# Performance work log

Measured on AMD Instinct MI355X. Metric: run time of the kernel, lower is better.

The kernel has to match this reference:

```python
import jax, jax.numpy as jnp
import numpy as np

DIM = 768
N_HEADS = 12
HEAD_DIM = DIM // N_HEADS  # 64
SEQ = 4096
ROPE_THETA = 10000.0  # local layer (layer_id=1)
WINDOW = 128          # local_attention; mask is distance <= WINDOW // 2


def setup_inputs() -> dict:
    key = jax.random.key(0)
    k1, k2, k3 = jax.random.split(key, 3)
    x = jax.random.normal(k1, (1, SEQ, DIM), dtype=jnp.float32)
    position_ids = jnp.arange(SEQ, dtype=jnp.int64 if jax.config.jax_enable_x64 else jnp.int32).reshape(1, SEQ)
    wqkv = jax.random.normal(k2, (3 * DIM, DIM), dtype=jnp.float32) * 0.02
    wo = jax.random.normal(k3, (DIM, DIM), dtype=jnp.float32) * 0.02
    return {"x": x, "position_ids": position_ids, "wqkv": wqkv, "wo": wo}


def _rope_cos_sin(position_ids):
    # inv_freq over even dims, freqs duplicated to full head_dim
    inv_freq = 1.0 / (ROPE_THETA ** (jnp.arange(0, HEAD_DIM, 2, dtype=jnp.float32) / HEAD_DIM))
    pos = position_ids.reshape(-1).astype(jnp.float32)           # [S]
    freqs = pos[:, None] * inv_freq[None, :]                      # [S, hd/2]
    freqs = jnp.concatenate([freqs, freqs], axis=-1)              # [S, hd]
    return jnp.cos(freqs)[None, None], jnp.sin(freqs)[None, None]  # [1,1,S,hd]


def _rotate_half(t):
    h = t.shape[-1] // 2
    return jnp.concatenate([-t[..., h:], t[..., :h]], axis=-1)


def reference(x, position_ids, wqkv, wo):
    bsz, seq_len, _ = x.shape
    qkv = jnp.einsum("bsd,ed->bse", x, wqkv)                      # [B,S,3*dim]
    qkv = qkv.reshape(bsz, seq_len, 3, N_HEADS, HEAD_DIM)
    qkv = jnp.transpose(qkv, (0, 3, 2, 1, 4))                      # [B,H,3,S,hd]
    q, k, v = qkv[:, :, 0], qkv[:, :, 1], qkv[:, :, 2]             # [B,H,S,hd]

    cos, sin = _rope_cos_sin(position_ids)
    q = q * cos + _rotate_half(q) * sin
    k = k * cos + _rotate_half(k) * sin

    scale = HEAD_DIM ** -0.5
    scores = jnp.einsum("bhqd,bhkd->bhqk", q, k) * scale           # [B,H,S,S]

    # sliding-window mask: |i - j| <= WINDOW // 2
    idx = jnp.arange(seq_len)
    dist = jnp.abs(idx[None, :] - idx[:, None])                    # [S,S]
    window_mask = dist <= (WINDOW // 2)
    scores = jnp.where(window_mask[None, None], scores, -jnp.inf)

    attn = jax.nn.softmax(scores, axis=-1)
    out = jnp.einsum("bhqk,bhkd->bhqd", attn, v)                   # [B,H,S,hd]
    out = jnp.transpose(out, (0, 2, 1, 3)).reshape(bsz, seq_len, DIM)
    out = jnp.einsum("bsd,ed->bse", out, wo)
    return out
```

## Files before the change

### kernel.cpp

```cpp
#include <hip/hip_runtime.h>
#include <math.h>

#define SEQ 4096
#define DIM 768
#define NH 12
#define HD 64
#define QKV_N 2304
#define HALF_WIN 64

typedef __attribute__((ext_vector_type(8))) short bf16x8;
typedef __attribute__((ext_vector_type(4))) float floatx4;

__device__ __forceinline__ unsigned short f2bf(float f) {
    unsigned u = __float_as_uint(f);
    unsigned r = (u + 0x7fffu + ((u >> 16) & 1u)) >> 16;
    return (unsigned short)r;
}

__device__ __forceinline__ void gld16(const void* g, void* l) {
    __builtin_amdgcn_global_load_lds(
        (const __attribute__((address_space(1))) unsigned*)g,
        (__attribute__((address_space(3))) unsigned*)l, 16, 0, 0);
}

__device__ __forceinline__ void fast_sc(float x, float* s, float* c) {
    float r = x * 0.15915494309189535f;
    r = r - floorf(r);
    *s = __builtin_amdgcn_sinf(r);
    *c = __builtin_amdgcn_cosf(r);
}

__global__ __launch_bounds__(256) void cast3_bf16(const float* __restrict__ x,
                                                  const float* __restrict__ wqkv,
                                                  const float* __restrict__ wo,
                                                  unsigned short* __restrict__ dst,
                                                  int nx4, int nw4, int ntot4) {
    int i = blockIdx.x * 256 + threadIdx.x;
    if (i >= ntot4) return;
    const float4* src;
    int off;
    if (i < nx4)            { src = (const float4*)x;    off = i; }
    else if (i < nx4 + nw4) { src = (const float4*)wqkv; off = i - nx4; }
    else                    { src = (const float4*)wo;   off = i - nx4 - nw4; }
    float4 v = src[off];
    ushort4 r;
    r.x = f2bf(v.x); r.y = f2bf(v.y); r.z = f2bf(v.z); r.w = f2bf(v.w);
    *(ushort4*)(dst + (size_t)i * 4) = r;
}

__global__ __launch_bounds__(256) void gemm_qkv_rope(const unsigned short* __restrict__ A,
                                                     const unsigned short* __restrict__ B,
                                                     unsigned short* __restrict__ qr,
                                                     unsigned short* __restrict__ kr,
                                                     unsigned short* __restrict__ vt) {
    __shared__ __align__(16) short smem[32768];
    const int t  = threadIdx.x;
    const int wv = t >> 6, ln = t & 63;
    const int wm = wv >> 1, wn = wv & 1;
    const int bm0 = blockIdx.y * 128;
    const int bn0 = blockIdx.x * 128;
    const int lrow = ln >> 3;
    const int lu   = ln & 7;
    const int frow = ln & 15;
    const int q    = ln >> 4;
    const int K = DIM;

    const unsigned short* gptr[8];
    int loff[8];
#pragma unroll
    for (int i = 0; i < 8; i++) {
        int idx = wv * 8 + i;
        int c   = (idx < 16) ? idx : idx - 16;
        int row = c * 8 + lrow;
        int g   = (lu ^ (row & 7)) << 3;
        if (idx < 16) {
            gptr[i] = A + (size_t)(bm0 + row) * K + g;
            loff[i] = c * 512;
        } else {
            gptr[i] = B + (size_t)(bn0 + row) * K + g;
            loff[i] = 8192 + c * 512;
        }
    }

    floatx4 acc[4][4];
#pragma unroll
    for (int i = 0; i < 4; i++)
#pragma unroll
        for (int j = 0; j < 4; j++) acc[i][j] = (floatx4){0.f, 0.f, 0.f, 0.f};

#pragma unroll
    for (int i = 0; i < 8; i++) gld16(gptr[i], (void*)(smem + loff[i]));
    __syncthreads();

    int cur = 0;
    for (int it = 0; it < 12; it++) {
        if (it + 1 < 12) {
            int nb = cur ^ 1;
            int k0n = (it + 1) * 64;
#pragma unroll
            for (int i = 0; i < 8; i++)
                gld16(gptr[i] + k0n, (void*)(smem + nb * 16384 + loff[i]));
        }
        short* As = smem + cur * 16384;
        short* Bs = As + 8192;
#pragma unroll
        for (int ks = 0; ks < 2; ks++) {
            bf16x8 af[4], bfr[4];
#pragma unroll
            for (int mt = 0; mt < 4; mt++) {
                int ra = wm * 64 + mt * 16 + frow;
                af[mt] = *(const bf16x8*)&As[ra * 64 + (((ks * 4 + q) ^ (ra & 7)) << 3)];
            }
#pragma unroll
            for (int nt = 0; nt < 4; nt++) {
                int rb = wn * 64 + nt * 16 + frow;
                bfr[nt] = *(const bf16x8*)&Bs[rb * 64 + (((ks * 4 + q) ^ (rb & 7)) << 3)];
            }
#pragma unroll
            for (int mt = 0; mt < 4; mt++)
#pragma unroll
                for (int nt = 0; nt < 4; nt++)
                    acc[mt][nt] = __builtin_amdgcn_mfma_f32_16x16x32_bf16(
                        af[mt], bfr[nt], acc[mt][nt], 0, 0, 0);
        }
        __syncthreads();
        cur ^= 1;
    }

    const int cn = frow;
    const int part = (bn0 >= 1536) ? 2 : (bn0 >= 768 ? 1 : 0);

    if (part < 2) {
        const int wcol = bn0 - part * 768 + wn * 64;
        const int h = wcol >> 6;
        unsigned short* dst = (part == 0 ? qr : kr) + (size_t)h * SEQ * HD;
        const float invf0 = exp2f(-(float)cn * 0.4152410118609203f);
        const float invf1 = exp2f(-(float)(cn + 16) * 0.4152410118609203f);
#pragma unroll
        for (int mt = 0; mt < 4; mt++) {
            const int sbase = bm0 + wm * 64 + mt * 16 + q * 4;
#pragma unroll
            for (int r = 0; r < 4; r++) {
                float ss = (float)(sbase + r);
                float sn0, cs0, sn1, cs1;
                fast_sc(ss * invf0, &sn0, &cs0);
                fast_sc(ss * invf1, &sn1, &cs1);
                float o0 = acc[mt][0][r] * cs0 - acc[mt][2][r] * sn0;
                float o1 = acc[mt][1][r] * cs1 - acc[mt][3][r] * sn1;
                float o2 = acc[mt][2][r] * cs0 + acc[mt][0][r] * sn0;
                float o3 = acc[mt][3][r] * cs1 + acc[mt][1][r] * sn1;
                unsigned short* p = dst + (size_t)(sbase + r) * HD + cn;
                p[0]  = f2bf(o0);
                p[16] = f2bf(o1);
                p[32] = f2bf(o2);
                p[48] = f2bf(o3);
            }
        }
    } else {
        short* vstage = smem + wv * 4608;
#pragma unroll
        for (int mt = 0; mt < 4; mt++) {
#pragma unroll
            for (int nt = 0; nt < 4; nt++) {
                int d    = nt * 16 + cn;
                int sloc = mt * 16 + q * 4;
                ushort4 pk;
                pk.x = f2bf(acc[mt][nt][0]);
                pk.y = f2bf(acc[mt][nt][1]);
                pk.z = f2bf(acc[mt][nt][2]);
                pk.w = f2bf(acc[mt][nt][3]);
                *(ushort4*)&vstage[d * 72 + sloc] = pk;
            }
        }
        __syncthreads();
#pragma unroll
        for (int itr = 0; itr < 8; itr++) {
            int dr = (t >> 4) + itr * 16;
            int u  = t & 15;
            int region = ((u >> 3) << 1) | (dr >> 6);
            uint4 val = *(const uint4*)&smem[region * 4608 + (dr & 63) * 72 + (u & 7) * 8];
            unsigned short* vp = vt + (size_t)(bn0 - 1536 + dr) * SEQ + bm0 + u * 8;
            *(uint4*)vp = val;
        }
    }
}

__global__ __launch_bounds__(256) void gemm_out(const unsigned short* __restrict__ A,
                                                const unsigned short* __restrict__ B,
                                                float* __restrict__ C,
                                                int M, int N, int K) {
    __shared__ __align__(16) short smem[16384];
    const int t  = threadIdx.x;
    const int wv = t >> 6, ln = t & 63;
    const int wm = wv >> 1, wn = wv & 1;
    const int bm0 = blockIdx.y * 64;
    const int bn0 = blockIdx.x * 64;
    const int lrow = ln >> 3;
    const int lu   = ln & 7;
    const int frow = ln & 15;
    const int q    = ln >> 4;

    const unsigned short* gptr[4];
    int loff[4];
#pragma unroll
    for (int i = 0; i < 4; i++) {
        int idx = wv * 4 + i;
        int c   = (idx < 8) ? idx : idx - 8;
        int row = c * 8 + lrow;
        int g   = (lu ^ (row & 7)) << 3;
        if (idx < 8) {
            gptr[i] = A + (size_t)(bm0 + row) * K + g;
            loff[i] = c * 512;
        } else {
            gptr[i] = B + (size_t)(bn0 + row) * K + g;
            loff[i] = 4096 + c * 512;
        }
    }

    floatx4 acc[2][2];
#pragma unroll
    for (int i = 0; i < 2; i++)
#pragma unroll
        for (int j = 0; j < 2; j++) acc[i][j] = (floatx4){0.f, 0.f, 0.f, 0.f};

#pragma unroll
    for (int i = 0; i < 4; i++) gld16(gptr[i], (void*)(smem + loff[i]));
    __syncthreads();

    int cur = 0;
    const int NIT = K / 64;
    for (int it = 0; it < NIT; it++) {
        if (it + 1 < NIT) {
            int nb = cur ^ 1;
            int k0n = (it + 1) * 64;
#pragma unroll
            for (int i = 0; i < 4; i++)
                gld16(gptr[i] + k0n, (void*)(smem + nb * 8192 + loff[i]));
        }
        short* As = smem + cur * 8192;
        short* Bs = As + 4096;
#pragma unroll
        for (int ks = 0; ks < 2; ks++) {
            bf16x8 af[2], bfr[2];
#pragma unroll
            for (int mt = 0; mt < 2; mt++) {
                int ra = wm * 32 + mt * 16 + frow;
                af[mt] = *(const bf16x8*)&As[ra * 64 + (((ks * 4 + q) ^ (ra & 7)) << 3)];
            }
#pragma unroll
            for (int nt = 0; nt < 2; nt++) {
                int rb = wn * 32 + nt * 16 + frow;
                bfr[nt] = *(const bf16x8*)&Bs[rb * 64 + (((ks * 4 + q) ^ (rb & 7)) << 3)];
            }
#pragma unroll
            for (int mt = 0; mt < 2; mt++)
#pragma unroll
                for (int nt = 0; nt < 2; nt++)
                    acc[mt][nt] = __builtin_amdgcn_mfma_f32_16x16x32_bf16(
                        af[mt], bfr[nt], acc[mt][nt], 0, 0, 0);
        }
        __syncthreads();
        cur ^= 1;
    }

    const int cn = ln & 15;
    const int rb4 = (ln >> 4) * 4;
#pragma unroll
    for (int mt = 0; mt < 2; mt++) {
#pragma unroll
        for (int nt = 0; nt < 2; nt++) {
            floatx4 v = acc[mt][nt];
            float* cp = C + (size_t)(bm0 + wm * 32 + mt * 16 + rb4) * N +
                        bn0 + wn * 32 + nt * 16 + cn;
#pragma unroll
            for (int r = 0; r < 4; r++) cp[(size_t)r * N] = v[r];
        }
    }
}

__global__ __launch_bounds__(512) void attn_mfma(const unsigned short* __restrict__ Q,
                                                 const unsigned short* __restrict__ K,
                                                 const unsigned short* __restrict__ Vt,
                                                 unsigned short* __restrict__ Out) {
    __shared__ __align__(16) short lds[16384];
    short* Ks  = lds;
    short* Vts = lds + 4096;
    short* Pb  = lds + 8192;
    const int t  = threadIdx.x;
    const int wv = t >> 6, ln = t & 63;
    const int h  = blockIdx.x, qs = blockIdx.y * 128;
    const int frow = ln & 15, qd = ln >> 4;
    const int rl = ln >> 3, uu = ln & 7;
    const unsigned short* Qh = Q + (size_t)h * SEQ * HD;
    const unsigned short* Kh = K + (size_t)h * SEQ * HD;
    const unsigned short* Vh = Vt + (size_t)h * HD * SEQ;

    const unsigned short* qp = Qh + (size_t)(qs + wv * 16 + frow) * HD;
    bf16x8 af0 = *(const bf16x8*)(qp + qd * 8);
    bf16x8 af1 = *(const bf16x8*)(qp + (qd + 4) * 8);

    floatx4 accO[4];
#pragma unroll
    for (int i = 0; i < 4; i++) accO[i] = (floatx4){0.f, 0.f, 0.f, 0.f};
    float m_r[4] = {-1e30f, -1e30f, -1e30f, -1e30f};
    float l_r[4] = {0.f, 0.f, 0.f, 0.f};

    const int qlo = wv * 16;

    for (int c = 0; c < 4; c++) {
        const int kb  = qs - 64 + c * 64;
        const int kbc = kb < 0 ? 0 : (kb > SEQ - 64 ? SEQ - 64 : kb);
        __syncthreads();
        {
            int row = wv * 8 + rl;
            int g = uu ^ ((row + (row >> 3)) & 7);
            gld16(Kh + (size_t)(kbc + row) * HD + g * 8, (void*)(Ks + wv * 512));
            gld16(Vh + (size_t)row * SEQ + kbc + g * 8, (void*)(Vts + wv * 512));
        }
        __syncthreads();

        const int klo0 = c * 64 - 64;
        bool live_kt[4];
        bool any_live = false;
#pragma unroll
        for (int kt = 0; kt < 4; kt++) {
            int d0 = qlo - (klo0 + kt * 16);
            live_kt[kt] = (d0 <= 64) && (d0 >= -64);
            any_live = any_live || live_kt[kt];
        }

        float sv[4][4];
        float cm[4] = {-1e30f, -1e30f, -1e30f, -1e30f};
        if (any_live) {
#pragma unroll
            for (int kt = 0; kt < 4; kt++) {
                if (live_kt[kt]) {
                    int brow = kt * 16 + frow;
                    int bz = (brow + (brow >> 3)) & 7;
                    bf16x8 b0 = *(const bf16x8*)&Ks[brow * 64 + ((qd ^ bz) << 3)];
                    bf16x8 b1 = *(const bf16x8*)&Ks[brow * 64 + (((qd + 4) ^ bz) << 3)];
                    floatx4 z = (floatx4){0.f, 0.f, 0.f, 0.f};
                    z = __builtin_amdgcn_mfma_f32_16x16x32_bf16(af0, b0, z, 0, 0, 0);
                    z = __builtin_amdgcn_mfma_f32_16x16x32_bf16(af1, b1, z, 0, 0, 0);
                    int gk = kb + kt * 16 + frow;
#pragma unroll
                    for (int r = 0; r < 4; r++) {
                        int gq = qs + wv * 16 + qd * 4 + r;
                        int dd = gq - gk;
                        bool valid = (gk >= 0) && (gk < SEQ) &&
                                     (dd <= HALF_WIN) && (dd >= -HALF_WIN);
                        float x = valid ? z[r] * 0.125f : -1e30f;
                        sv[kt][r] = x;
                        cm[r] = fmaxf(cm[r], x);
                    }
                } else {
#pragma unroll
                    for (int r = 0; r < 4; r++) sv[kt][r] = -1e30f;
                }
            }
#pragma unroll
            for (int off = 1; off < 16; off <<= 1)
#pragma unroll
                for (int r = 0; r < 4; r++)
                    cm[r] = fmaxf(cm[r], __shfl_xor(cm[r], off, 64));
            float al[4], ls[4];
#pragma unroll
            for (int r = 0; r < 4; r++) {
                float mn = fmaxf(m_r[r], cm[r]);
                al[r] = __expf(m_r[r] - mn);
                m_r[r] = mn;
                ls[r] = 0.f;
            }
            const int qrb = wv * 16 + qd * 4;
#pragma unroll
            for (int kt = 0; kt < 4; kt++) {
                int klocal = kt * 16 + frow;
                int ku = klocal >> 3;
                if (live_kt[kt]) {
#pragma unroll
                    for (int r = 0; r < 4; r++) {
                        float p = (sv[kt][r] > -1e29f) ? __expf(sv[kt][r] - m_r[r]) : 0.f;
                        ls[r] += p;
                        int qrow = qrb + r;
                        int pz = (qrow + (qrow >> 3)) & 7;
                        Pb[qrow * 64 + ((ku ^ pz) << 3) + (klocal & 7)] = (short)f2bf(p);
                    }
                } else {
#pragma unroll
                    for (int r = 0; r < 4; r++) {
                        int qrow = qrb + r;
                        int pz = (qrow + (qrow >> 3)) & 7;
                        Pb[qrow * 64 + ((ku ^ pz) << 3) + (klocal & 7)] = 0;
                    }
                }
            }
#pragma unroll
            for (int off = 1; off < 16; off <<= 1)
#pragma unroll
                for (int r = 0; r < 4; r++) ls[r] += __shfl_xor(ls[r], off, 64);
#pragma unroll
            for (int r = 0; r < 4; r++) l_r[r] = l_r[r] * al[r] + ls[r];
#pragma unroll
            for (int dt = 0; dt < 4; dt++)
#pragma unroll
                for (int r = 0; r < 4; r++) accO[dt][r] *= al[r];
        }
        __syncthreads();

        if (any_live) {
            const int prow = wv * 16 + frow;
            const int pz2 = (prow + (prow >> 3)) & 7;
            bf16x8 pa0 = *(const bf16x8*)&Pb[prow * 64 + ((qd ^ pz2) << 3)];
            bf16x8 pa1 = *(const bf16x8*)&Pb[prow * 64 + (((qd + 4) ^ pz2) << 3)];
#pragma unroll
            for (int dt = 0; dt < 4; dt++) {
                int vrow = dt * 16 + frow;
                int vz = (vrow + (vrow >> 3)) & 7;
                bf16x8 v0 = *(const bf16x8*)&Vts[vrow * 64 + ((qd ^ vz) << 3)];
                bf16x8 v1 = *(const bf16x8*)&Vts[vrow * 64 + (((qd + 4) ^ vz) << 3)];
                accO[dt] = __builtin_amdgcn_mfma_f32_16x16x32_bf16(pa0, v0, accO[dt], 0, 0, 0);
                accO[dt] = __builtin_amdgcn_mfma_f32_16x16x32_bf16(pa1, v1, accO[dt], 0, 0, 0);
            }
        }
    }

    __syncthreads();
    short* Ob = lds;
    float linv[4];
#pragma unroll
    for (int r = 0; r < 4; r++) linv[r] = 1.0f / l_r[r];
#pragma unroll
    for (int dt = 0; dt < 4; dt++)
#pragma unroll
        for (int r = 0; r < 4; r++) {
            int qrow = wv * 16 + qd * 4 + r;
            int dcol = dt * 16 + frow;
            Ob[qrow * 72 + dcol] = (short)f2bf(accO[dt][r] * linv[r]);
        }
    __syncthreads();
    const int orow = t >> 2, og = (t & 3) * 16;
    uint4 a = *(const uint4*)&Ob[orow * 72 + og];
    uint4 b = *(const uint4*)&Ob[orow * 72 + og + 8];
    unsigned short* op = Out + (size_t)(qs + orow) * DIM + h * HD + og;
    *(uint4*)(op)     = a;
    *(uint4*)(op + 8) = b;
}

extern "C" void kernel_launch(void* const* d_in, const int* in_sizes, int n_in,
                              void* d_out, int out_size, void* d_ws, size_t ws_size,
                              hipStream_t stream) {
    const float* x    = (const float*)d_in[0];
    const float* wqkv = (const float*)d_in[2];
    const float* wo   = (const float*)d_in[3];
    float* out = (float*)d_out;

    unsigned short* q_r  = (unsigned short*)d_ws;
    unsigned short* k_r  = q_r + (size_t)NH * SEQ * HD;
    unsigned short* v_t  = k_r + (size_t)NH * SEQ * HD;
    unsigned short* x_bf = v_t + (size_t)NH * SEQ * HD;
    unsigned short* wqkv_bf = x_bf + (size_t)SEQ * DIM;
    unsigned short* wo_bf   = wqkv_bf + (size_t)QKV_N * DIM;
    unsigned short* attn_bf = wo_bf + (size_t)DIM * DIM;

    const int nx4 = SEQ * DIM / 4;
    const int nw4 = QKV_N * DIM / 4;
    const int no4 = DIM * DIM / 4;
    const int ntot4 = nx4 + nw4 + no4;

    cast3_bf16<<<dim3((ntot4 + 255) / 256), 256, 0, stream>>>(
        x, wqkv, wo, x_bf, nx4, nw4, ntot4);
    gemm_qkv_rope<<<dim3(QKV_N / 128, SEQ / 128), 256, 0, stream>>>(
        x_bf, wqkv_bf, q_r, k_r, v_t);
    attn_mfma<<<dim3(NH, SEQ / 128), 512, 0, stream>>>(
        q_r, k_r, v_t, attn_bf);
    gemm_out<<<dim3(DIM / 64, SEQ / 64), 256, 0, stream>>>(
        attn_bf, wo_bf, out, SEQ, DIM, DIM);
}
```

Baseline: 127.0 us.

## Restructure sliding-window attention to per-wave single-pass softmax with direct global K/V loads

```diff
diff --git a/kernel.cpp b/kernel.cpp
--- a/kernel.cpp
+++ b/kernel.cpp
@@ -278,164 +278,106 @@
     }
 }
 
-__global__ __launch_bounds__(512) void attn_mfma(const unsigned short* __restrict__ Q,
+#define QBLK 64
+#define PBS 170
+
+__global__ __launch_bounds__(256) void attn_mfma(const unsigned short* __restrict__ Q,
                                                  const unsigned short* __restrict__ K,
                                                  const unsigned short* __restrict__ Vt,
                                                  unsigned short* __restrict__ Out) {
     __shared__ __align__(16) short lds[16384];
-    short* Ks  = lds;
-    short* Vts = lds + 4096;
-    short* Pb  = lds + 8192;
+    short* Pb = lds;
+    short* Ob = lds + 10880;
     const int t  = threadIdx.x;
     const int wv = t >> 6, ln = t & 63;
-    const int h  = blockIdx.x, qs = blockIdx.y * 128;
+    const int h  = blockIdx.x, qs = blockIdx.y * QBLK;
     const int frow = ln & 15, qd = ln >> 4;
-    const int rl = ln >> 3, uu = ln & 7;
     const unsigned short* Qh = Q + (size_t)h * SEQ * HD;
     const unsigned short* Kh = K + (size_t)h * SEQ * HD;
     const unsigned short* Vh = Vt + (size_t)h * HD * SEQ;
 
-    const unsigned short* qp = Qh + (size_t)(qs + wv * 16 + frow) * HD;
+    const int gq0 = qs + wv * 16;
+    const int t0  = (gq0 >> 4) - 4;
+    short* Pw = Pb + wv * 16 * PBS;
+
+    const unsigned short* qp = Qh + (size_t)(gq0 + frow) * HD;
     bf16x8 af0 = *(const bf16x8*)(qp + qd * 8);
     bf16x8 af1 = *(const bf16x8*)(qp + (qd + 4) * 8);
 
+    float sv[9][4];
+    float cm[4] = {-1e30f, -1e30f, -1e30f, -1e30f};
+#pragma unroll
+    for (int i = 0; i < 9; i++) {
+        int kt = t0 + i;
+        if (kt >= 0 && kt < SEQ / 16) {
+            int kk = kt * 16;
+            const unsigned short* kp = Kh + (size_t)(kk + frow) * HD;
+            bf16x8 b0 = *(const bf16x8*)(kp + qd * 8);
+            bf16x8 b1 = *(const bf16x8*)(kp + (qd + 4) * 8);
+            floatx4 z = (floatx4){0.f, 0.f, 0.f, 0.f};
+            z = __builtin_amdgcn_mfma_f32_16x16x32_bf16(af0, b0, z, 0, 0, 0);
+            z = __builtin_amdgcn_mfma_f32_16x16x32_bf16(af1, b1, z, 0, 0, 0);
+            int gk = kk + frow;
+#pragma unroll
+            for (int r = 0; r < 4; r++) {
+                int dd = gq0 + qd * 4 + r - gk;
+                bool valid = (dd <= HALF_WIN) && (dd >= -HALF_WIN);
+                float x = valid ? z[r] * 0.125f : -1e30f;
+                sv[i][r] = x;
+                cm[r] = fmaxf(cm[r], x);
+            }
+        } else {
+#pragma unroll
+            for (int r = 0; r < 4; r++) sv[i][r] = -1e30f;
+        }
+    }
+#pragma unroll
+    for (int off = 1; off < 16; off <<= 1)
+#pragma unroll
+        for (int r = 0; r < 4; r++) cm[r] = fmaxf(cm[r], __shfl_xor(cm[r], off, 64));
+
+    float ls[4] = {0.f, 0.f, 0.f, 0.f};
+#pragma unroll
+    for (int i = 0; i < 9; i++) {
+#pragma unroll
+        for (int r = 0; r < 4; r++) {
+            float p = __expf(sv[i][r] - cm[r]);
+            ls[r] += p;
+            Pw[(qd * 4 + r) * PBS + i * 16 + frow] = (short)f2bf(p);
+        }
+    }
+#pragma unroll
+    for (int r = 0; r < 4; r++) Pw[(qd * 4 + r) * PBS + 144 + frow] = 0;
+#pragma unroll
+    for (int off = 1; off < 16; off <<= 1)
+#pragma unroll
+        for (int r = 0; r < 4; r++) ls[r] += __shfl_xor(ls[r], off, 64);
+
     floatx4 accO[4];
 #pragma unroll
     for (int i = 0; i < 4; i++) accO[i] = (floatx4){0.f, 0.f, 0.f, 0.f};
-    float m_r[4] = {-1e30f, -1e30f, -1e30f, -1e30f};
-    float l_r[4] = {0.f, 0.f, 0.f, 0.f};
-
-    const int qlo = wv * 16;
-
-    for (int c = 0; c < 4; c++) {
-        const int kb  = qs - 64 + c * 64;
-        const int kbc = kb < 0 ? 0 : (kb > SEQ - 64 ? SEQ - 64 : kb);
-        __syncthreads();
-        {
-            int row = wv * 8 + rl;
-            int g = uu ^ ((row + (row >> 3)) & 7);
-            gld16(Kh + (size_t)(kbc + row) * HD + g * 8, (void*)(Ks + wv * 512));
-            gld16(Vh + (size_t)row * SEQ + kbc + g * 8, (void*)(Vts + wv * 512));
-        }
-        __syncthreads();
-
-        const int klo0 = c * 64 - 64;
-        bool live_kt[4];
-        bool any_live = false;
-#pragma unroll
-        for (int kt = 0; kt < 4; kt++) {
-            int d0 = qlo - (klo0 + kt * 16);
-            live_kt[kt] = (d0 <= 64) && (d0 >= -64);
-            any_live = any_live || live_kt[kt];
-        }
-
-        float sv[4][4];
-        float cm[4] = {-1e30f, -1e30f, -1e30f, -1e30f};
-        if (any_live) {
-#pragma unroll
-            for (int kt = 0; kt < 4; kt++) {
-                if (live_kt[kt]) {
-                    int brow = kt * 16 + frow;
-                    int bz = (brow + (brow >> 3)) & 7;
-                    bf16x8 b0 = *(const bf16x8*)&Ks[brow * 64 + ((qd ^ bz) << 3)];
-                    bf16x8 b1 = *(const bf16x8*)&Ks[brow * 64 + (((qd + 4) ^ bz) << 3)];
-                    floatx4 z = (floatx4){0.f, 0.f, 0.f, 0.f};
-                    z = __builtin_amdgcn_mfma_f32_16x16x32_bf16(af0, b0, z, 0, 0, 0);
-                    z = __builtin_amdgcn_mfma_f32_16x16x32_bf16(af1, b1, z, 0, 0, 0);
-                    int gk = kb + kt * 16 + frow;
-#pragma unroll
-                    for (int r = 0; r < 4; r++) {
-                        int gq = qs + wv * 16 + qd * 4 + r;
-                        int dd = gq - gk;
-                        bool valid = (gk >= 0) && (gk < SEQ) &&
-                                     (dd <= HALF_WIN) && (dd >= -HALF_WIN);
-                        float x = valid ? z[r] * 0.125f : -1e30f;
-                        sv[kt][r] = x;
-                        cm[r] = fmaxf(cm[r], x);
-                    }
-                } else {
-#pragma unroll
-                    for (int r = 0; r < 4; r++) sv[kt][r] = -1e30f;
-                }
-            }
-#pragma unroll
-            for (int off = 1; off < 16; off <<= 1)
-#pragma unroll
-                for (int r = 0; r < 4; r++)
-                    cm[r] = fmaxf(cm[r], __shfl_xor(cm[r], off, 64));
-            float al[4], ls[4];
-#pragma unroll
-            for (int r = 0; r < 4; r++) {
-                float mn = fmaxf(m_r[r], cm[r]);
-                al[r] = __expf(m_r[r] - mn);
-                m_r[r] = mn;
-                ls[r] = 0.f;
-            }
-            const int qrb = wv * 16 + qd * 4;
-#pragma unroll
-            for (int kt = 0; kt < 4; kt++) {
-                int klocal = kt * 16 + frow;
-                int ku = klocal >> 3;
-                if (live_kt[kt]) {
-#pragma unroll
-                    for (int r = 0; r < 4; r++) {
-                        float p = (sv[kt][r] > -1e29f) ? __expf(sv[kt][r] - m_r[r]) : 0.f;
-                        ls[r] += p;
-                        int qrow = qrb + r;
-                        int pz = (qrow + (qrow >> 3)) & 7;
-                        Pb[qrow * 64 + ((ku ^ pz) << 3) + (klocal & 7)] = (short)f2bf(p);
-                    }
-                } else {
-#pragma unroll
-                    for (int r = 0; r < 4; r++) {
-                        int qrow = qrb + r;
-                        int pz = (qrow + (qrow >> 3)) & 7;
-                        Pb[qrow * 64 + ((ku ^ pz) << 3) + (klocal & 7)] = 0;
-                    }
-                }
-            }
-#pragma unroll
-            for (int off = 1; off < 16; off <<= 1)
-#pragma unroll
-                for (int r = 0; r < 4; r++) ls[r] += __shfl_xor(ls[r], off, 64);
-#pragma unroll
-            for (int r = 0; r < 4; r++) l_r[r] = l_r[r] * al[r] + ls[r];
-#pragma unroll
-            for (int dt = 0; dt < 4; dt++)
-#pragma unroll
-                for (int r = 0; r < 4; r++) accO[dt][r] *= al[r];
-        }
-        __syncthreads();
-
-        if (any_live) {
-            const int prow = wv * 16 + frow;
-            const int pz2 = (prow + (prow >> 3)) & 7;
-            bf16x8 pa0 = *(const bf16x8*)&Pb[prow * 64 + ((qd ^ pz2) << 3)];
-            bf16x8 pa1 = *(const bf16x8*)&Pb[prow * 64 + (((qd + 4) ^ pz2) << 3)];
-#pragma unroll
-            for (int dt = 0; dt < 4; dt++) {
-                int vrow = dt * 16 + frow;
-                int vz = (vrow + (vrow >> 3)) & 7;
-                bf16x8 v0 = *(const bf16x8*)&Vts[vrow * 64 + ((qd ^ vz) << 3)];
-                bf16x8 v1 = *(const bf16x8*)&Vts[vrow * 64 + (((qd + 4) ^ vz) << 3)];
-                accO[dt] = __builtin_amdgcn_mfma_f32_16x16x32_bf16(pa0, v0, accO[dt], 0, 0, 0);
-                accO[dt] = __builtin_amdgcn_mfma_f32_16x16x32_bf16(pa1, v1, accO[dt], 0, 0, 0);
-            }
-        }
-    }
-
-    __syncthreads();
-    short* Ob = lds;
+    const int kbase = t0 * 16;
+#pragma unroll
+    for (int g = 0; g < 5; g++) {
+        bf16x8 pa = *(const bf16x8*)&Pw[frow * PBS + g * 32 + qd * 8];
+        int key = kbase + g * 32 + qd * 8;
+        key = key < 0 ? 0 : (key > SEQ - 8 ? SEQ - 8 : key);
+#pragma unroll
+        for (int dt = 0; dt < 4; dt++) {
+            bf16x8 v = *(const bf16x8*)(Vh + (size_t)(dt * 16 + frow) * SEQ + key);
+            accO[dt] = __builtin_amdgcn_mfma_f32_16x16x32_bf16(pa, v, accO[dt], 0, 0, 0);
+        }
+    }
+
     float linv[4];
 #pragma unroll
-    for (int r = 0; r < 4; r++) linv[r] = 1.0f / l_r[r];
+    for (int r = 0; r < 4; r++) linv[r] = 1.0f / ls[r];
 #pragma unroll
     for (int dt = 0; dt < 4; dt++)
 #pragma unroll
         for (int r = 0; r < 4; r++) {
             int qrow = wv * 16 + qd * 4 + r;
-            int dcol = dt * 16 + frow;
-            Ob[qrow * 72 + dcol] = (short)f2bf(accO[dt][r] * linv[r]);
+            Ob[qrow * 72 + dt * 16 + frow] = (short)f2bf(accO[dt][r] * linv[r]);
         }
     __syncthreads();
     const int orow = t >> 2, og = (t & 3) * 16;
@@ -471,7 +413,7 @@
         x, wqkv, wo, x_bf, nx4, nw4, ntot4);
     gemm_qkv_rope<<<dim3(QKV_N / 128, SEQ / 128), 256, 0, stream>>>(
         x_bf, wqkv_bf, q_r, k_r, v_t);
-    attn_mfma<<<dim3(NH, SEQ / 128), 512, 0, stream>>>(
+    attn_mfma<<<dim3(NH, SEQ / QBLK), 256, 0, stream>>>(
         q_r, k_r, v_t, attn_bf);
     gemm_out<<<dim3(DIM / 64, SEQ / 64), 256, 0, stream>>>(
         attn_bf, wo_bf, out, SEQ, DIM, DIM);
```

Result: slower. 133.0 us (+4.8%).
